# Optimization experiments

Hardware: AMD Instinct MI355X
Metric: run time of the kernel (lower is better)

Reference implementation:

```python
import jax, jax.numpy as jnp
import numpy as np

D_MODEL = 1024
NUM_HEADS = 16
HEAD_DIM = D_MODEL // NUM_HEADS

def setup_inputs() -> dict:
    key = jax.random.key(0)
    ks = jax.random.split(key, 9)
    B, L = 2, 2048
    s = 1.0 / np.sqrt(D_MODEL)
    return {
        "x":  jax.random.normal(ks[0], (B, L, D_MODEL), dtype=jnp.float32),
        "Wq": jax.random.uniform(ks[1], (D_MODEL, D_MODEL), jnp.float32, -s, s),
        "bq": jax.random.uniform(ks[2], (D_MODEL,), jnp.float32, -s, s),
        "Wk": jax.random.uniform(ks[3], (D_MODEL, D_MODEL), jnp.float32, -s, s),
        "bk": jax.random.uniform(ks[4], (D_MODEL,), jnp.float32, -s, s),
        "Wv": jax.random.uniform(ks[5], (D_MODEL, D_MODEL), jnp.float32, -s, s),
        "bv": jax.random.uniform(ks[6], (D_MODEL,), jnp.float32, -s, s),
        "Wo": jax.random.uniform(ks[7], (D_MODEL, D_MODEL), jnp.float32, -s, s),
        "bo": jax.random.uniform(ks[8], (D_MODEL,), jnp.float32, -s, s),
    }

def _split_heads(t):
    B, L, _ = t.shape
    return t.reshape(B, L, NUM_HEADS, HEAD_DIM).transpose(0, 2, 1, 3)  # [B,H,L,Dh]

def reference(x, Wq, bq, Wk, bk, Wv, bv, Wo, bo):
    # Linear projections (torch Linear: y = x @ W.T + b)
    Q = _split_heads(x @ Wq.T + bq)
    K = _split_heads(x @ Wk.T + bk)
    V = _split_heads(x @ Wv.T + bv)
    scale = 1.0 / jnp.sqrt(jnp.asarray(HEAD_DIM, dtype=x.dtype))
    scores = jnp.einsum('bhqd,bhkd->bhqk', Q, K) * scale  # [B,H,L,L]
    attn_weights = jax.nn.softmax(scores, axis=-1)
    ctx = jnp.einsum('bhqk,bhkd->bhqd', attn_weights, V)  # [B,H,L,Dh]
    B, H, L, Dh = ctx.shape
    ctx = ctx.transpose(0, 2, 1, 3).reshape(B, L, H * Dh)
    out = ctx @ Wo.T + bo  # dropout p=0.0 -> identity
    return (out, attn_weights)
```

## Files before the change

kernel.cpp:

```cpp
#include <hip/hip_runtime.h>

typedef unsigned short u16;
typedef __bf16 bf16x8 __attribute__((ext_vector_type(8)));
typedef float f32x4 __attribute__((ext_vector_type(4)));

#define WSTR 72
#define TSZ (64 * WSTR)

__device__ __forceinline__ u16 f2bf(float f) {
    union { float f; unsigned int u; } v; v.f = f;
    unsigned int u = v.u;
    u += 0x7fffu + ((u >> 16) & 1u);
    return (u16)(u >> 16);
}

__device__ __forceinline__ u16 cvt_bf(float f) {
    __bf16 h = (__bf16)f;
    union { __bf16 h; u16 u; } v; v.h = h; return v.u;
}

__device__ __forceinline__ void gload16(const u16* g, u16* l) {
    __builtin_amdgcn_global_load_lds((const __attribute__((address_space(1))) unsigned int*)(const void*)g,
                                     (__attribute__((address_space(3))) unsigned int*)(void*)l, 16, 0, 0);
}

#define MFMA16(A, B, C) __builtin_amdgcn_mfma_f32_16x16x32_bf16(A, B, C, 0, 0, 0)

#define LGKM_BARRIER() do { \
    asm volatile("s_waitcnt lgkmcnt(0)\n\ts_barrier" ::: "memory"); \
    __builtin_amdgcn_sched_barrier(0); \
} while (0)

__global__ __launch_bounds__(256) void k_cvtX(const float* __restrict__ src, u16* __restrict__ dst) {
    const size_t i = ((size_t)blockIdx.x * 256 + threadIdx.x) * 8;
    float4 v0 = *(const float4*)(src + i);
    float4 v1 = *(const float4*)(src + i + 4);
    u16 o[8];
    o[0] = f2bf(v0.x); o[1] = f2bf(v0.y); o[2] = f2bf(v0.z); o[3] = f2bf(v0.w);
    o[4] = f2bf(v1.x); o[5] = f2bf(v1.y); o[6] = f2bf(v1.z); o[7] = f2bf(v1.w);
    *(uint4*)(dst + i) = *(const uint4*)o;
}

__global__ __launch_bounds__(256) void k_cvtW(const float* __restrict__ w0, const float* __restrict__ w1,
                                              const float* __restrict__ w2, const float* __restrict__ w3,
                                              u16* __restrict__ dst) {
    const int z = blockIdx.z;
    const float* src = z == 0 ? w0 : z == 1 ? w1 : z == 2 ? w2 : w3;
    const size_t i = ((size_t)blockIdx.x * 256 + threadIdx.x) * 8;
    float4 v0 = *(const float4*)(src + i);
    float4 v1 = *(const float4*)(src + i + 4);
    u16 o[8];
    o[0] = f2bf(v0.x); o[1] = f2bf(v0.y); o[2] = f2bf(v0.z); o[3] = f2bf(v0.w);
    o[4] = f2bf(v1.x); o[5] = f2bf(v1.y); o[6] = f2bf(v1.z); o[7] = f2bf(v1.w);
    *(uint4*)(dst + (size_t)z * 1048576 + i) = *(const uint4*)o;
}

__global__ __launch_bounds__(256) void k_qkv(const u16* __restrict__ Xb, const u16* __restrict__ Wb,
                                             const float* __restrict__ bq, const float* __restrict__ bk,
                                             const float* __restrict__ bv,
                                             u16* __restrict__ Q, u16* __restrict__ Kd, u16* __restrict__ Vt) {
    __shared__ __align__(16) u16 lA[128 * 32];
    __shared__ __align__(16) u16 lB[128 * 32];
    __shared__ __align__(16) u16 lE[128 * 72];
    const int t = threadIdx.x;
    const int n0 = blockIdx.x * 128;
    const int m0 = blockIdx.y * 128;
    const int lane = t & 63, wave = t >> 6;
    const int wm = (wave >> 1) * 64, wn = (wave & 1) * 64;
    const int quad = lane >> 4, m16 = lane & 15;
    const int r4 = t >> 2, c8 = (t & 3) * 8;
    f32x4 acc[4][4] = {};
    for (int k0 = 0; k0 < 1024; k0 += 32) {
        gload16(Xb + (size_t)(m0 + r4) * 1024 + k0 + c8,       &lA[t * 8]);
        gload16(Xb + (size_t)(m0 + 64 + r4) * 1024 + k0 + c8,  &lA[2048 + t * 8]);
        gload16(Wb + (size_t)(n0 + r4) * 1024 + k0 + c8,       &lB[t * 8]);
        gload16(Wb + (size_t)(n0 + 64 + r4) * 1024 + k0 + c8,  &lB[2048 + t * 8]);
        __syncthreads();
        bf16x8 af[4], bfr[4];
#pragma unroll
        for (int i = 0; i < 4; ++i) {
            af[i]  = *(const bf16x8*)(lA + (wm + i * 16 + m16) * 32 + quad * 8);
            bfr[i] = *(const bf16x8*)(lB + (wn + i * 16 + m16) * 32 + quad * 8);
        }
#pragma unroll
        for (int mi = 0; mi < 4; ++mi)
#pragma unroll
            for (int ni = 0; ni < 4; ++ni)
                acc[mi][ni] = MFMA16(af[mi], bfr[ni], acc[mi][ni]);
        __syncthreads();
    }
    const int b = m0 >> 11, l0 = m0 & 2047;
#pragma unroll
    for (int hx = 0; hx < 2; ++hx) {
        __syncthreads();
        if ((wave & 1) == hx) {
#pragma unroll
            for (int ni = 0; ni < 4; ++ni) {
                const int col = n0 + wn + ni * 16 + m16;
                const int mat = col >> 10;
                const float bias = (mat == 0 ? bq : mat == 1 ? bk : bv)[col & 1023];
#pragma unroll
                for (int mi = 0; mi < 4; ++mi)
#pragma unroll
                    for (int e = 0; e < 4; ++e)
                        lE[(wm + mi * 16 + quad * 4 + e) * 72 + ni * 16 + m16] = cvt_bf(acc[mi][ni][e] + bias);
            }
        }
        __syncthreads();
        const int gb = n0 + hx * 64;
        const int mat = gb >> 10, h = (gb & 1023) >> 6;
        const int bh = b * 16 + h;
        if (mat < 2) {
            u16* dst = (mat == 0 ? Q : Kd) + (((size_t)bh * 2048) + l0) * 64;
            const int r = t >> 1, off = (t & 1) * 32;
            const u16* s = lE + r * 72 + off;
            u16* d2 = dst + (size_t)r * 64 + off;
            *(uint4*)(d2 + 0)  = *(const uint4*)(s + 0);
            *(uint4*)(d2 + 8)  = *(const uint4*)(s + 8);
            *(uint4*)(d2 + 16) = *(const uint4*)(s + 16);
            *(uint4*)(d2 + 24) = *(const uint4*)(s + 24);
        } else {
            const int d = t >> 2, ch = t & 3;
            u16* dst = Vt + ((size_t)bh * 64 + d) * 2048 + l0 + ch * 32;
#pragma unroll
            for (int seg = 0; seg < 4; ++seg) {
                u16 p[8];
#pragma unroll
                for (int j = 0; j < 8; ++j) p[j] = lE[(ch * 32 + seg * 8 + j) * 72 + d];
                *(uint4*)(dst + seg * 8) = *(const uint4*)p;
            }
        }
    }
}

__global__ __launch_bounds__(256) void k_attn(const u16* __restrict__ Q,
                                              const u16* __restrict__ K,
                                              const u16* __restrict__ Vt,
                                              float* __restrict__ attn,
                                              u16* __restrict__ ctx) {
    __shared__ __align__(16) u16 lK[2 * TSZ];
    __shared__ __align__(16) u16 lV[2 * TSZ];
    __shared__ __align__(16) u16 lW[2 * TSZ];
    __shared__ float sred[2][64];
    const int t = threadIdx.x;
    const int bh = blockIdx.x;
    const int m0 = blockIdx.y * 64;
    const int lane = t & 63, wave = t >> 6;
    const int wq = (wave & 1) * 32;
    const int wk = (wave >> 1) * 32;
    const int wm = (wave >> 1) * 32, wn = (wave & 1) * 32;
    const int quad = lane >> 4, m16 = lane & 15;
    const int sr = t >> 3, sc = (t & 7) * 8;
    const u16* Qh = Q + (size_t)bh * 2048 * 64;
    const u16* Kh = K + (size_t)bh * 2048 * 64;
    const u16* Vh = Vt + (size_t)bh * 64 * 2048;
    float* ah = attn + ((size_t)bh << 22) + (size_t)m0 * 2048;

    const float SC = 0.18033688011112042f;

    bf16x8 qf[2][2];
#pragma unroll
    for (int ni = 0; ni < 2; ++ni)
#pragma unroll
        for (int ks = 0; ks < 2; ++ks)
            qf[ni][ks] = *(const bf16x8*)(Qh + (size_t)(m0 + wq + ni * 16 + m16) * 64 + ks * 32 + quad * 8);

    float slane[2] = {0.f, 0.f};
    {
        *(uint4*)&lK[sr * WSTR + sc]        = *(const uint4*)(Kh + (size_t)sr * 64 + sc);
        *(uint4*)&lK[(sr + 32) * WSTR + sc] = *(const uint4*)(Kh + (size_t)(sr + 32) * 64 + sc);
        int buf = 0;
        for (int kt = 0; kt < 32; ++kt) {
            LGKM_BARRIER();
            uint4 kr0, kr1;
            if (kt < 31) {
                const u16* kp = Kh + (size_t)(kt + 1) * 64 * 64;
                kr0 = *(const uint4*)(kp + (size_t)sr * 64 + sc);
                kr1 = *(const uint4*)(kp + (size_t)(sr + 32) * 64 + sc);
            }
            const u16* lKb = &lK[buf * TSZ];
            bf16x8 k00 = *(const bf16x8*)(lKb + (wk + m16) * WSTR + quad * 8);
            bf16x8 k01 = *(const bf16x8*)(lKb + (wk + m16) * WSTR + 32 + quad * 8);
            bf16x8 k10 = *(const bf16x8*)(lKb + (wk + 16 + m16) * WSTR + quad * 8);
            bf16x8 k11 = *(const bf16x8*)(lKb + (wk + 16 + m16) * WSTR + 32 + quad * 8);
            f32x4 sacc[2][2] = {};
            __builtin_amdgcn_s_setprio(1);
            sacc[0][0] = MFMA16(k00, qf[0][0], sacc[0][0]);
            sacc[0][1] = MFMA16(k00, qf[1][0], sacc[0][1]);
            sacc[1][0] = MFMA16(k10, qf[0][0], sacc[1][0]);
            sacc[1][1] = MFMA16(k10, qf[1][0], sacc[1][1]);
            sacc[0][0] = MFMA16(k01, qf[0][1], sacc[0][0]);
            sacc[0][1] = MFMA16(k01, qf[1][1], sacc[0][1]);
            sacc[1][0] = MFMA16(k11, qf[0][1], sacc[1][0]);
            sacc[1][1] = MFMA16(k11, qf[1][1], sacc[1][1]);
            __builtin_amdgcn_s_setprio(0);
#pragma unroll
            for (int mi = 0; mi < 2; ++mi)
#pragma unroll
                for (int e = 0; e < 4; ++e) {
                    slane[0] += __builtin_amdgcn_exp2f(sacc[mi][0][e] * SC);
                    slane[1] += __builtin_amdgcn_exp2f(sacc[mi][1][e] * SC);
                }
            if (kt < 31) {
                u16* dK = &lK[(buf ^ 1) * TSZ];
                *(uint4*)&dK[sr * WSTR + sc]        = kr0;
                *(uint4*)&dK[(sr + 32) * WSTR + sc] = kr1;
            }
            buf ^= 1;
        }
    }
#pragma unroll
    for (int ni = 0; ni < 2; ++ni) {
        slane[ni] += __shfl_xor(slane[ni], 16);
        slane[ni] += __shfl_xor(slane[ni], 32);
    }
    __syncthreads();
    if (quad == 0) {
        sred[wave >> 1][wq + m16]      = slane[0];
        sred[wave >> 1][wq + 16 + m16] = slane[1];
    }
    __syncthreads();
    float inv[2];
    inv[0] = 1.0f / (sred[0][wq + m16]      + sred[1][wq + m16]);
    inv[1] = 1.0f / (sred[0][wq + 16 + m16] + sred[1][wq + 16 + m16]);

    unsigned aoff[2][2], lwoff[2][2];
#pragma unroll
    for (int mi = 0; mi < 2; ++mi)
#pragma unroll
        for (int ni = 0; ni < 2; ++ni) {
            const int q = wq + ni * 16 + m16;
            const int k = wk + mi * 16 + quad * 4;
            aoff[mi][ni]  = (unsigned)(q * 2048 + k);
            lwoff[mi][ni] = (unsigned)(q * WSTR + k);
        }

    f32x4 cacc[2][2] = {};
    bf16x8 vp00 = {}, vp01 = {}, vp10 = {}, vp11 = {};
    {
        *(uint4*)&lK[sr * WSTR + sc]        = *(const uint4*)(Kh + (size_t)sr * 64 + sc);
        *(uint4*)&lK[(sr + 32) * WSTR + sc] = *(const uint4*)(Kh + (size_t)(sr + 32) * 64 + sc);
        *(uint4*)&lV[sr * WSTR + sc]        = *(const uint4*)(Vh + (size_t)sr * 2048 + sc);
        *(uint4*)&lV[(sr + 32) * WSTR + sc] = *(const uint4*)(Vh + (size_t)(sr + 32) * 2048 + sc);
        int buf = 0;
        for (int kt = 0; kt < 32; ++kt) {
            LGKM_BARRIER();
            uint4 kr0, kr1, vr0, vr1;
            if (kt < 31) {
                const u16* kp  = Kh + (size_t)(kt + 1) * 64 * 64;
                const u16* vp2 = Vh + (size_t)(kt + 1) * 64;
                kr0 = *(const uint4*)(kp + (size_t)sr * 64 + sc);
                kr1 = *(const uint4*)(kp + (size_t)(sr + 32) * 64 + sc);
                vr0 = *(const uint4*)(vp2 + (size_t)sr * 2048 + sc);
                vr1 = *(const uint4*)(vp2 + (size_t)(sr + 32) * 2048 + sc);
            }
            const u16* lKb = &lK[buf * TSZ];
            const u16* lVb = &lV[buf * TSZ];
            bf16x8 vn00 = *(const bf16x8*)(lVb + (wn + m16) * WSTR + quad * 8);
            bf16x8 vn01 = *(const bf16x8*)(lVb + (wn + m16) * WSTR + 32 + quad * 8);
            bf16x8 vn10 = *(const bf16x8*)(lVb + (wn + 16 + m16) * WSTR + quad * 8);
            bf16x8 vn11 = *(const bf16x8*)(lVb + (wn + 16 + m16) * WSTR + 32 + quad * 8);
            bf16x8 k00 = *(const bf16x8*)(lKb + (wk + m16) * WSTR + quad * 8);
            bf16x8 k01 = *(const bf16x8*)(lKb + (wk + m16) * WSTR + 32 + quad * 8);
            bf16x8 k10 = *(const bf16x8*)(lKb + (wk + 16 + m16) * WSTR + quad * 8);
            bf16x8 k11 = *(const bf16x8*)(lKb + (wk + 16 + m16) * WSTR + 32 + quad * 8);
            f32x4 sacc[2][2] = {};
            __builtin_amdgcn_s_setprio(1);
            sacc[0][0] = MFMA16(k00, qf[0][0], sacc[0][0]);
            sacc[0][1] = MFMA16(k00, qf[1][0], sacc[0][1]);
            sacc[1][0] = MFMA16(k10, qf[0][0], sacc[1][0]);
            sacc[1][1] = MFMA16(k10, qf[1][0], sacc[1][1]);
            sacc[0][0] = MFMA16(k01, qf[0][1], sacc[0][0]);
            sacc[0][1] = MFMA16(k01, qf[1][1], sacc[0][1]);
            sacc[1][0] = MFMA16(k11, qf[0][1], sacc[1][0]);
            sacc[1][1] = MFMA16(k11, qf[1][1], sacc[1][1]);
            __builtin_amdgcn_s_setprio(0);
#pragma unroll
            for (int mi = 0; mi < 2; ++mi)
#pragma unroll
                for (int ni = 0; ni < 2; ++ni)
#pragma unroll
                    for (int e = 0; e < 4; ++e)
                        sacc[mi][ni][e] = __builtin_amdgcn_exp2f(sacc[mi][ni][e] * SC) * inv[ni];
            u16* lwb = &lW[(kt & 1) * TSZ];
#pragma unroll
            for (int mi = 0; mi < 2; ++mi)
#pragma unroll
                for (int ni = 0; ni < 2; ++ni) {
                    u16 p[4];
                    p[0] = cvt_bf(sacc[mi][ni][0]); p[1] = cvt_bf(sacc[mi][ni][1]);
                    p[2] = cvt_bf(sacc[mi][ni][2]); p[3] = cvt_bf(sacc[mi][ni][3]);
                    *(uint2*)&lwb[lwoff[mi][ni]] = *(const uint2*)p;
                }
            float* ap = ah + kt * 64;
#pragma unroll
            for (int mi = 0; mi < 2; ++mi)
#pragma unroll
                for (int ni = 0; ni < 2; ++ni)
                    *(f32x4*)(ap + aoff[mi][ni]) = sacc[mi][ni];
            if (kt < 31) {
                u16* dK = &lK[(buf ^ 1) * TSZ];
                u16* dV = &lV[(buf ^ 1) * TSZ];
                *(uint4*)&dK[sr * WSTR + sc]        = kr0;
                *(uint4*)&dK[(sr + 32) * WSTR + sc] = kr1;
                *(uint4*)&dV[sr * WSTR + sc]        = vr0;
                *(uint4*)&dV[(sr + 32) * WSTR + sc] = vr1;
            }
            if (kt > 0) {
                const u16* lwp = &lW[((kt - 1) & 1) * TSZ];
                bf16x8 a00 = *(const bf16x8*)(lwp + (wm + m16) * WSTR + quad * 8);
                bf16x8 a01 = *(const bf16x8*)(lwp + (wm + m16) * WSTR + 32 + quad * 8);
                bf16x8 a10 = *(const bf16x8*)(lwp + (wm + 16 + m16) * WSTR + quad * 8);
                bf16x8 a11 = *(const bf16x8*)(lwp + (wm + 16 + m16) * WSTR + 32 + quad * 8);
                __builtin_amdgcn_s_setprio(1);
                cacc[0][0] = MFMA16(a00, vp00, cacc[0][0]);
                cacc[0][1] = MFMA16(a00, vp10, cacc[0][1]);
                cacc[1][0] = MFMA16(a10, vp00, cacc[1][0]);
                cacc[1][1] = MFMA16(a10, vp10, cacc[1][1]);
                cacc[0][0] = MFMA16(a01, vp01, cacc[0][0]);
                cacc[0][1] = MFMA16(a01, vp11, cacc[0][1]);
                cacc[1][0] = MFMA16(a11, vp01, cacc[1][0]);
                cacc[1][1] = MFMA16(a11, vp11, cacc[1][1]);
                __builtin_amdgcn_s_setprio(0);
            }
            vp00 = vn00; vp01 = vn01; vp10 = vn10; vp11 = vn11;
            buf ^= 1;
        }
        __syncthreads();
        const u16* lwp = &lW[(31 & 1) * TSZ];
        bf16x8 a00 = *(const bf16x8*)(lwp + (wm + m16) * WSTR + quad * 8);
        bf16x8 a01 = *(const bf16x8*)(lwp + (wm + m16) * WSTR + 32 + quad * 8);
        bf16x8 a10 = *(const bf16x8*)(lwp + (wm + 16 + m16) * WSTR + quad * 8);
        bf16x8 a11 = *(const bf16x8*)(lwp + (wm + 16 + m16) * WSTR + 32 + quad * 8);
        cacc[0][0] = MFMA16(a00, vp00, cacc[0][0]);
        cacc[0][1] = MFMA16(a00, vp10, cacc[0][1]);
        cacc[1][0] = MFMA16(a10, vp00, cacc[1][0]);
        cacc[1][1] = MFMA16(a10, vp10, cacc[1][1]);
        cacc[0][0] = MFMA16(a01, vp01, cacc[0][0]);
        cacc[0][1] = MFMA16(a01, vp11, cacc[0][1]);
        cacc[1][0] = MFMA16(a11, vp01, cacc[1][0]);
        cacc[1][1] = MFMA16(a11, vp11, cacc[1][1]);
    }

    const int b = bh >> 4, h = bh & 15;
    u16* cp = ctx + ((size_t)b * 2048) * 1024 + h * 64;
#pragma unroll
    for (int mi = 0; mi < 2; ++mi)
#pragma unroll
        for (int ni = 0; ni < 2; ++ni)
#pragma unroll
            for (int e = 0; e < 4; ++e) {
                const int row = m0 + wm + mi * 16 + quad * 4 + e;
                const int col = wn + ni * 16 + m16;
                cp[(size_t)row * 1024 + col] = cvt_bf(cacc[mi][ni][e]);
            }
}

__global__ __launch_bounds__(256) void k_out(const u16* __restrict__ ctx,
                                             const u16* __restrict__ WoB,
                                             const float* __restrict__ bo,
                                             float* __restrict__ out) {
    __shared__ __align__(16) u16 lA[128 * 32];
    __shared__ __align__(16) u16 lB[128 * 32];
    const int t = threadIdx.x;
    const int n0 = blockIdx.x * 128;
    const int m0 = blockIdx.y * 128;
    const int lane = t & 63, wave = t >> 6;
    const int wm = (wave >> 1) * 64, wn = (wave & 1) * 64;
    const int quad = lane >> 4, m16 = lane & 15;
    const int r4 = t >> 2, c8 = (t & 3) * 8;
    f32x4 acc[4][4] = {};
    for (int k0 = 0; k0 < 1024; k0 += 32) {
        gload16(ctx + (size_t)(m0 + r4) * 1024 + k0 + c8,       &lA[t * 8]);
        gload16(ctx + (size_t)(m0 + 64 + r4) * 1024 + k0 + c8,  &lA[2048 + t * 8]);
        gload16(WoB + (size_t)(n0 + r4) * 1024 + k0 + c8,       &lB[t * 8]);
        gload16(WoB + (size_t)(n0 + 64 + r4) * 1024 + k0 + c8,  &lB[2048 + t * 8]);
        __syncthreads();
        bf16x8 af[4], bfr[4];
#pragma unroll
        for (int i = 0; i < 4; ++i) {
            af[i]  = *(const bf16x8*)(lA + (wm + i * 16 + m16) * 32 + quad * 8);
            bfr[i] = *(const bf16x8*)(lB + (wn + i * 16 + m16) * 32 + quad * 8);
        }
#pragma unroll
        for (int mi = 0; mi < 4; ++mi)
#pragma unroll
            for (int ni = 0; ni < 4; ++ni)
                acc[mi][ni] = MFMA16(af[mi], bfr[ni], acc[mi][ni]);
        __syncthreads();
    }
#pragma unroll
    for (int ni = 0; ni < 4; ++ni) {
        const int col = n0 + wn + ni * 16 + m16;
        const float bv = bo[col];
#pragma unroll
        for (int mi = 0; mi < 4; ++mi)
#pragma unroll
            for (int e = 0; e < 4; ++e) {
                const int row = m0 + wm + mi * 16 + quad * 4 + e;
                out[(size_t)row * 1024 + col] = acc[mi][ni][e] + bv;
            }
    }
}

extern "C" void kernel_launch(void* const* d_in, const int* in_sizes, int n_in,
                              void* d_out, int out_size, void* d_ws, size_t ws_size,
                              hipStream_t stream) {
    const float* x  = (const float*)d_in[0];
    const float* Wq = (const float*)d_in[1];
    const float* bq = (const float*)d_in[2];
    const float* Wk = (const float*)d_in[3];
    const float* bk = (const float*)d_in[4];
    const float* Wv = (const float*)d_in[5];
    const float* bv = (const float*)d_in[6];
    const float* Wo = (const float*)d_in[7];
    const float* bo = (const float*)d_in[8];

    float* out_f = (float*)d_out;
    float* attn  = out_f + (size_t)4096 * 1024;

    u16* Xb = (u16*)d_ws;
    u16* Wb = Xb + (size_t)4194304;
    u16* Qb = Wb + (size_t)4194304;
    u16* Kb = Qb + (size_t)4194304;
    u16* Vt = Kb + (size_t)4194304;

    dim3 blk(256);
    k_cvtX<<<dim3(2048), blk, 0, stream>>>(x, Xb);
    k_cvtW<<<dim3(512, 1, 4), blk, 0, stream>>>(Wq, Wk, Wv, Wo, Wb);
    k_qkv<<<dim3(24, 32), blk, 0, stream>>>(Xb, Wb, bq, bk, bv, Qb, Kb, Vt);
    k_attn<<<dim3(32, 32), blk, 0, stream>>>(Qb, Kb, Vt, attn, Xb);
    k_out<<<dim3(8, 32), blk, 0, stream>>>(Xb, Wb + (size_t)3072 * 1024, bo, out_f);
}
```

Baseline: 702.5 us.

## Split softmax row-sum pass into separate kernel with larger key tiles

Moves the first pass of attention (computing the exp row sums) out of the attention kernel into its own kernel, which gives each wave 64 query rows and 32 keys per 128-key tile so K loads are reused across more queries and fewer loop iterations are needed. The inverse sums are written to a scratch region in the output buffer, reusing the out area that k_out later overwrites, and the second kernel reads them back. The second kernel also drops the s_setprio hints around its MFMA blocks. The cost is an extra kernel launch plus a small global round trip for the normalizers, and the second kernel's smaller shared-memory footprint may change occupancy.

```diff
diff --git a/kernel.cpp b/kernel.cpp
--- a/kernel.cpp
+++ b/kernel.cpp
@@ -6,6 +6,7 @@
 
 #define WSTR 72
 #define TSZ (64 * WSTR)
+#define KTSZ (128 * WSTR)
 
 __device__ __forceinline__ u16 f2bf(float f) {
     union { float f; unsigned int u; } v; v.f = f;
@@ -133,15 +134,99 @@
     }
 }
 
-__global__ __launch_bounds__(256) void k_attn(const u16* __restrict__ Q,
-                                              const u16* __restrict__ K,
-                                              const u16* __restrict__ Vt,
-                                              float* __restrict__ attn,
-                                              u16* __restrict__ ctx) {
+__global__ __launch_bounds__(256) void k_sum(const u16* __restrict__ Q,
+                                             const u16* __restrict__ K,
+                                             float* __restrict__ invg) {
+    __shared__ __align__(16) u16 lK[2 * KTSZ];
+    __shared__ float sred[4][64];
+    const int t = threadIdx.x;
+    const int bh = blockIdx.x;
+    const int m0 = blockIdx.y * 64;
+    const int lane = t & 63, wave = t >> 6;
+    const int wk = wave * 32;
+    const int quad = lane >> 4, m16 = lane & 15;
+    const int sr = t >> 3, sc = (t & 7) * 8;
+    const u16* Qh = Q + (size_t)bh * 2048 * 64;
+    const u16* Kh = K + (size_t)bh * 2048 * 64;
+    const float SC = 0.18033688011112042f;
+
+    bf16x8 qf[4][2];
+#pragma unroll
+    for (int ni = 0; ni < 4; ++ni)
+#pragma unroll
+        for (int ks = 0; ks < 2; ++ks)
+            qf[ni][ks] = *(const bf16x8*)(Qh + (size_t)(m0 + ni * 16 + m16) * 64 + ks * 32 + quad * 8);
+
+    float slane[4] = {0.f, 0.f, 0.f, 0.f};
+#pragma unroll
+    for (int g = 0; g < 4; ++g)
+        *(uint4*)&lK[(sr + g * 32) * WSTR + sc] = *(const uint4*)(Kh + (size_t)(sr + g * 32) * 64 + sc);
+    int buf = 0;
+    for (int kt = 0; kt < 16; ++kt) {
+        LGKM_BARRIER();
+        uint4 kr[4];
+        if (kt < 15) {
+            const u16* kp = Kh + (size_t)(kt + 1) * 128 * 64;
+#pragma unroll
+            for (int g = 0; g < 4; ++g)
+                kr[g] = *(const uint4*)(kp + (size_t)(sr + g * 32) * 64 + sc);
+        }
+        const u16* lKb = &lK[buf * KTSZ];
+        bf16x8 kf[2][2];
+#pragma unroll
+        for (int mi = 0; mi < 2; ++mi)
+#pragma unroll
+            for (int ks = 0; ks < 2; ++ks)
+                kf[mi][ks] = *(const bf16x8*)(lKb + (wk + mi * 16 + m16) * WSTR + ks * 32 + quad * 8);
+        f32x4 sacc[2][4] = {};
+#pragma unroll
+        for (int ks = 0; ks < 2; ++ks)
+#pragma unroll
+            for (int ni = 0; ni < 4; ++ni) {
+                sacc[0][ni] = MFMA16(kf[0][ks], qf[ni][ks], sacc[0][ni]);
+                sacc[1][ni] = MFMA16(kf[1][ks], qf[ni][ks], sacc[1][ni]);
+            }
+#pragma unroll
+        for (int ni = 0; ni < 4; ++ni)
+#pragma unroll
+            for (int mi = 0; mi < 2; ++mi)
+#pragma unroll
+                for (int e = 0; e < 4; ++e)
+                    slane[ni] += __builtin_amdgcn_exp2f(sacc[mi][ni][e] * SC);
+        if (kt < 15) {
+            u16* dK = &lK[(buf ^ 1) * KTSZ];
+#pragma unroll
+            for (int g = 0; g < 4; ++g)
+                *(uint4*)&dK[(sr + g * 32) * WSTR + sc] = kr[g];
+        }
+        buf ^= 1;
+    }
+#pragma unroll
+    for (int ni = 0; ni < 4; ++ni) {
+        slane[ni] += __shfl_xor(slane[ni], 16);
+        slane[ni] += __shfl_xor(slane[ni], 32);
+    }
+    if (quad == 0) {
+#pragma unroll
+        for (int ni = 0; ni < 4; ++ni)
+            sred[wave][ni * 16 + m16] = slane[ni];
+    }
+    __syncthreads();
+    if (t < 64) {
+        const float s = (sred[0][t] + sred[1][t]) + (sred[2][t] + sred[3][t]);
+        invg[(size_t)bh * 2048 + m0 + t] = 1.0f / s;
+    }
+}
+
+__global__ __launch_bounds__(256) void k_wpv(const u16* __restrict__ Q,
+                                             const u16* __restrict__ K,
+                                             const u16* __restrict__ Vt,
+                                             const float* __restrict__ invg,
+                                             float* __restrict__ attn,
+                                             u16* __restrict__ ctx) {
     __shared__ __align__(16) u16 lK[2 * TSZ];
     __shared__ __align__(16) u16 lV[2 * TSZ];
     __shared__ __align__(16) u16 lW[2 * TSZ];
-    __shared__ float sred[2][64];
     const int t = threadIdx.x;
     const int bh = blockIdx.x;
     const int m0 = blockIdx.y * 64;
@@ -155,7 +240,6 @@
     const u16* Kh = K + (size_t)bh * 2048 * 64;
     const u16* Vh = Vt + (size_t)bh * 64 * 2048;
     float* ah = attn + ((size_t)bh << 22) + (size_t)m0 * 2048;
-
     const float SC = 0.18033688011112042f;
 
     bf16x8 qf[2][2];
@@ -165,64 +249,9 @@
         for (int ks = 0; ks < 2; ++ks)
             qf[ni][ks] = *(const bf16x8*)(Qh + (size_t)(m0 + wq + ni * 16 + m16) * 64 + ks * 32 + quad * 8);
 
-    float slane[2] = {0.f, 0.f};
-    {
-        *(uint4*)&lK[sr * WSTR + sc]        = *(const uint4*)(Kh + (size_t)sr * 64 + sc);
-        *(uint4*)&lK[(sr + 32) * WSTR + sc] = *(const uint4*)(Kh + (size_t)(sr + 32) * 64 + sc);
-        int buf = 0;
-        for (int kt = 0; kt < 32; ++kt) {
-            LGKM_BARRIER();
-            uint4 kr0, kr1;
-            if (kt < 31) {
-                const u16* kp = Kh + (size_t)(kt + 1) * 64 * 64;
-                kr0 = *(const uint4*)(kp + (size_t)sr * 64 + sc);
-                kr1 = *(const uint4*)(kp + (size_t)(sr + 32) * 64 + sc);
-            }
-            const u16* lKb = &lK[buf * TSZ];
-            bf16x8 k00 = *(const bf16x8*)(lKb + (wk + m16) * WSTR + quad * 8);
-            bf16x8 k01 = *(const bf16x8*)(lKb + (wk + m16) * WSTR + 32 + quad * 8);
-            bf16x8 k10 = *(const bf16x8*)(lKb + (wk + 16 + m16) * WSTR + quad * 8);
-            bf16x8 k11 = *(const bf16x8*)(lKb + (wk + 16 + m16) * WSTR + 32 + quad * 8);
-            f32x4 sacc[2][2] = {};
-            __builtin_amdgcn_s_setprio(1);
-            sacc[0][0] = MFMA16(k00, qf[0][0], sacc[0][0]);
-            sacc[0][1] = MFMA16(k00, qf[1][0], sacc[0][1]);
-            sacc[1][0] = MFMA16(k10, qf[0][0], sacc[1][0]);
-            sacc[1][1] = MFMA16(k10, qf[1][0], sacc[1][1]);
-            sacc[0][0] = MFMA16(k01, qf[0][1], sacc[0][0]);
-            sacc[0][1] = MFMA16(k01, qf[1][1], sacc[0][1]);
-            sacc[1][0] = MFMA16(k11, qf[0][1], sacc[1][0]);
-            sacc[1][1] = MFMA16(k11, qf[1][1], sacc[1][1]);
-            __builtin_amdgcn_s_setprio(0);
-#pragma unroll
-            for (int mi = 0; mi < 2; ++mi)
-#pragma unroll
-                for (int e = 0; e < 4; ++e) {
-                    slane[0] += __builtin_amdgcn_exp2f(sacc[mi][0][e] * SC);
-                    slane[1] += __builtin_amdgcn_exp2f(sacc[mi][1][e] * SC);
-                }
-            if (kt < 31) {
-                u16* dK = &lK[(buf ^ 1) * TSZ];
-                *(uint4*)&dK[sr * WSTR + sc]        = kr0;
-                *(uint4*)&dK[(sr + 32) * WSTR + sc] = kr1;
-            }
-            buf ^= 1;
-        }
-    }
-#pragma unroll
-    for (int ni = 0; ni < 2; ++ni) {
-        slane[ni] += __shfl_xor(slane[ni], 16);
-        slane[ni] += __shfl_xor(slane[ni], 32);
-    }
-    __syncthreads();
-    if (quad == 0) {
-        sred[wave >> 1][wq + m16]      = slane[0];
-        sred[wave >> 1][wq + 16 + m16] = slane[1];
-    }
-    __syncthreads();
     float inv[2];
-    inv[0] = 1.0f / (sred[0][wq + m16]      + sred[1][wq + m16]);
-    inv[1] = 1.0f / (sred[0][wq + 16 + m16] + sred[1][wq + 16 + m16]);
+    inv[0] = invg[(size_t)bh * 2048 + m0 + wq + m16];
+    inv[1] = invg[(size_t)bh * 2048 + m0 + wq + 16 + m16];
 
     unsigned aoff[2][2], lwoff[2][2];
 #pragma unroll
@@ -265,7 +294,6 @@
             bf16x8 k10 = *(const bf16x8*)(lKb + (wk + 16 + m16) * WSTR + quad * 8);
             bf16x8 k11 = *(const bf16x8*)(lKb + (wk + 16 + m16) * WSTR + 32 + quad * 8);
             f32x4 sacc[2][2] = {};
-            __builtin_amdgcn_s_setprio(1);
             sacc[0][0] = MFMA16(k00, qf[0][0], sacc[0][0]);
             sacc[0][1] = MFMA16(k00, qf[1][0], sacc[0][1]);
             sacc[1][0] = MFMA16(k10, qf[0][0], sacc[1][0]);
@@ -274,7 +302,6 @@
             sacc[0][1] = MFMA16(k01, qf[1][1], sacc[0][1]);
             sacc[1][0] = MFMA16(k11, qf[0][1], sacc[1][0]);
             sacc[1][1] = MFMA16(k11, qf[1][1], sacc[1][1]);
-            __builtin_amdgcn_s_setprio(0);
 #pragma unroll
             for (int mi = 0; mi < 2; ++mi)
 #pragma unroll
@@ -312,7 +339,6 @@
                 bf16x8 a01 = *(const bf16x8*)(lwp + (wm + m16) * WSTR + 32 + quad * 8);
                 bf16x8 a10 = *(const bf16x8*)(lwp + (wm + 16 + m16) * WSTR + quad * 8);
                 bf16x8 a11 = *(const bf16x8*)(lwp + (wm + 16 + m16) * WSTR + 32 + quad * 8);
-                __builtin_amdgcn_s_setprio(1);
                 cacc[0][0] = MFMA16(a00, vp00, cacc[0][0]);
                 cacc[0][1] = MFMA16(a00, vp10, cacc[0][1]);
                 cacc[1][0] = MFMA16(a10, vp00, cacc[1][0]);
@@ -321,7 +347,6 @@
                 cacc[0][1] = MFMA16(a01, vp11, cacc[0][1]);
                 cacc[1][0] = MFMA16(a11, vp01, cacc[1][0]);
                 cacc[1][1] = MFMA16(a11, vp11, cacc[1][1]);
-                __builtin_amdgcn_s_setprio(0);
             }
             vp00 = vn00; vp01 = vn01; vp10 = vn10; vp11 = vn11;
             buf ^= 1;
@@ -418,6 +443,7 @@
 
     float* out_f = (float*)d_out;
     float* attn  = out_f + (size_t)4096 * 1024;
+    float* invg  = out_f;
 
     u16* Xb = (u16*)d_ws;
     u16* Wb = Xb + (size_t)4194304;
@@ -429,6 +455,7 @@
     k_cvtX<<<dim3(2048), blk, 0, stream>>>(x, Xb);
     k_cvtW<<<dim3(512, 1, 4), blk, 0, stream>>>(Wq, Wk, Wv, Wo, Wb);
     k_qkv<<<dim3(24, 32), blk, 0, stream>>>(Xb, Wb, bq, bk, bv, Qb, Kb, Vt);
-    k_attn<<<dim3(32, 32), blk, 0, stream>>>(Qb, Kb, Vt, attn, Xb);
+    k_sum<<<dim3(32, 32), blk, 0, stream>>>(Qb, Kb, invg);
+    k_wpv<<<dim3(32, 32), blk, 0, stream>>>(Qb, Kb, Vt, invg, attn, Xb);
     k_out<<<dim3(8, 32), blk, 0, stream>>>(Xb, Wb + (size_t)3072 * 1024, bo, out_f);
 }
```

Measured after the change: 714.8 us. Within noise of the previous version (+1.8%).

## Stage K/V tiles via direct global-to-LDS loads with XOR-swizzled layout

Applied to the files above, without the earlier changes.

Replaces register-staged K and V tile copies in the attention kernel with global_load_lds direct-to-LDS loads into an unpadded buffer. Bank conflicts are avoided by XOR-swizzling the column index instead of padding. Barriers now wait on vmcnt, with vmcnt(8) in the second pass so the outstanding attention-weight stores need not drain. The s_setprio hints around MFMA blocks are removed. This removes VGPR staging and the extra ds_write instructions, at the cost of relying on correct vmcnt accounting for the store and load ordering.

```diff
diff --git a/kernel.cpp b/kernel.cpp
--- a/kernel.cpp
+++ b/kernel.cpp
@@ -6,6 +6,9 @@
 
 #define WSTR 72
 #define TSZ (64 * WSTR)
+#define KBUF 4096
+
+#define SWZ(r, e) ((r) * 64 + ((e) ^ (((r) & 7) * 8)))
 
 __device__ __forceinline__ u16 f2bf(float f) {
     union { float f; unsigned int u; } v; v.f = f;
@@ -26,8 +29,12 @@
 
 #define MFMA16(A, B, C) __builtin_amdgcn_mfma_f32_16x16x32_bf16(A, B, C, 0, 0, 0)
 
-#define LGKM_BARRIER() do { \
-    asm volatile("s_waitcnt lgkmcnt(0)\n\ts_barrier" ::: "memory"); \
+#define BAR_V0() do { \
+    asm volatile("s_waitcnt vmcnt(0) lgkmcnt(0)\n\ts_barrier" ::: "memory"); \
+    __builtin_amdgcn_sched_barrier(0); \
+} while (0)
+#define BAR_V8() do { \
+    asm volatile("s_waitcnt vmcnt(8) lgkmcnt(0)\n\ts_barrier" ::: "memory"); \
     __builtin_amdgcn_sched_barrier(0); \
 } while (0)
 
@@ -138,8 +145,8 @@
                                               const u16* __restrict__ Vt,
                                               float* __restrict__ attn,
                                               u16* __restrict__ ctx) {
-    __shared__ __align__(16) u16 lK[2 * TSZ];
-    __shared__ __align__(16) u16 lV[2 * TSZ];
+    __shared__ __align__(16) u16 lK[2 * KBUF];
+    __shared__ __align__(16) u16 lV[2 * KBUF];
     __shared__ __align__(16) u16 lW[2 * TSZ];
     __shared__ float sred[2][64];
     const int t = threadIdx.x;
@@ -150,13 +157,18 @@
     const int wk = (wave >> 1) * 32;
     const int wm = (wave >> 1) * 32, wn = (wave & 1) * 32;
     const int quad = lane >> 4, m16 = lane & 15;
-    const int sr = t >> 3, sc = (t & 7) * 8;
     const u16* Qh = Q + (size_t)bh * 2048 * 64;
     const u16* Kh = K + (size_t)bh * 2048 * 64;
     const u16* Vh = Vt + (size_t)bh * 64 * 2048;
     float* ah = attn + ((size_t)bh << 22) + (size_t)m0 * 2048;
-
     const float SC = 0.18033688011112042f;
+
+    const int sr2 = t >> 3, su = t & 7;
+    const int lu = su ^ (sr2 & 7);
+    const u16* Ksrc0 = Kh + (size_t)sr2 * 64 + lu * 8;
+    const u16* Ksrc1 = Kh + (size_t)(sr2 + 32) * 64 + lu * 8;
+    const u16* Vsrc0 = Vh + (size_t)sr2 * 2048 + lu * 8;
+    const u16* Vsrc1 = Vh + (size_t)(sr2 + 32) * 2048 + lu * 8;
 
     bf16x8 qf[2][2];
 #pragma unroll
@@ -167,24 +179,22 @@
 
     float slane[2] = {0.f, 0.f};
     {
-        *(uint4*)&lK[sr * WSTR + sc]        = *(const uint4*)(Kh + (size_t)sr * 64 + sc);
-        *(uint4*)&lK[(sr + 32) * WSTR + sc] = *(const uint4*)(Kh + (size_t)(sr + 32) * 64 + sc);
+        gload16(Ksrc0, &lK[t * 8]);
+        gload16(Ksrc1, &lK[2048 + t * 8]);
         int buf = 0;
         for (int kt = 0; kt < 32; ++kt) {
-            LGKM_BARRIER();
-            uint4 kr0, kr1;
+            BAR_V0();
             if (kt < 31) {
-                const u16* kp = Kh + (size_t)(kt + 1) * 64 * 64;
-                kr0 = *(const uint4*)(kp + (size_t)sr * 64 + sc);
-                kr1 = *(const uint4*)(kp + (size_t)(sr + 32) * 64 + sc);
-            }
-            const u16* lKb = &lK[buf * TSZ];
-            bf16x8 k00 = *(const bf16x8*)(lKb + (wk + m16) * WSTR + quad * 8);
-            bf16x8 k01 = *(const bf16x8*)(lKb + (wk + m16) * WSTR + 32 + quad * 8);
-            bf16x8 k10 = *(const bf16x8*)(lKb + (wk + 16 + m16) * WSTR + quad * 8);
-            bf16x8 k11 = *(const bf16x8*)(lKb + (wk + 16 + m16) * WSTR + 32 + quad * 8);
+                u16* dK = &lK[(buf ^ 1) * KBUF];
+                gload16(Ksrc0 + (size_t)(kt + 1) * 4096, &dK[t * 8]);
+                gload16(Ksrc1 + (size_t)(kt + 1) * 4096, &dK[2048 + t * 8]);
+            }
+            const u16* lKb = &lK[buf * KBUF];
+            bf16x8 k00 = *(const bf16x8*)(lKb + SWZ(wk + m16,      quad * 8));
+            bf16x8 k01 = *(const bf16x8*)(lKb + SWZ(wk + m16,      32 + quad * 8));
+            bf16x8 k10 = *(const bf16x8*)(lKb + SWZ(wk + 16 + m16, quad * 8));
+            bf16x8 k11 = *(const bf16x8*)(lKb + SWZ(wk + 16 + m16, 32 + quad * 8));
             f32x4 sacc[2][2] = {};
-            __builtin_amdgcn_s_setprio(1);
             sacc[0][0] = MFMA16(k00, qf[0][0], sacc[0][0]);
             sacc[0][1] = MFMA16(k00, qf[1][0], sacc[0][1]);
             sacc[1][0] = MFMA16(k10, qf[0][0], sacc[1][0]);
@@ -193,7 +203,6 @@
             sacc[0][1] = MFMA16(k01, qf[1][1], sacc[0][1]);
             sacc[1][0] = MFMA16(k11, qf[0][1], sacc[1][0]);
             sacc[1][1] = MFMA16(k11, qf[1][1], sacc[1][1]);
-            __builtin_amdgcn_s_setprio(0);
 #pragma unroll
             for (int mi = 0; mi < 2; ++mi)
 #pragma unroll
@@ -201,11 +210,6 @@
                     slane[0] += __builtin_amdgcn_exp2f(sacc[mi][0][e] * SC);
                     slane[1] += __builtin_amdgcn_exp2f(sacc[mi][1][e] * SC);
                 }
-            if (kt < 31) {
-                u16* dK = &lK[(buf ^ 1) * TSZ];
-                *(uint4*)&dK[sr * WSTR + sc]        = kr0;
-                *(uint4*)&dK[(sr + 32) * WSTR + sc] = kr1;
-            }
             buf ^= 1;
         }
     }
@@ -238,34 +242,33 @@
     f32x4 cacc[2][2] = {};
     bf16x8 vp00 = {}, vp01 = {}, vp10 = {}, vp11 = {};
     {
-        *(uint4*)&lK[sr * WSTR + sc]        = *(const uint4*)(Kh + (size_t)sr * 64 + sc);
-        *(uint4*)&lK[(sr + 32) * WSTR + sc] = *(const uint4*)(Kh + (size_t)(sr + 32) * 64 + sc);
-        *(uint4*)&lV[sr * WSTR + sc]        = *(const uint4*)(Vh + (size_t)sr * 2048 + sc);
-        *(uint4*)&lV[(sr + 32) * WSTR + sc] = *(const uint4*)(Vh + (size_t)(sr + 32) * 2048 + sc);
+        gload16(Ksrc0, &lK[t * 8]);
+        gload16(Ksrc1, &lK[2048 + t * 8]);
+        gload16(Vsrc0, &lV[t * 8]);
+        gload16(Vsrc1, &lV[2048 + t * 8]);
+        asm volatile("s_waitcnt vmcnt(0)" ::: "memory");
         int buf = 0;
         for (int kt = 0; kt < 32; ++kt) {
-            LGKM_BARRIER();
-            uint4 kr0, kr1, vr0, vr1;
+            BAR_V8();
             if (kt < 31) {
-                const u16* kp  = Kh + (size_t)(kt + 1) * 64 * 64;
-                const u16* vp2 = Vh + (size_t)(kt + 1) * 64;
-                kr0 = *(const uint4*)(kp + (size_t)sr * 64 + sc);
-                kr1 = *(const uint4*)(kp + (size_t)(sr + 32) * 64 + sc);
-                vr0 = *(const uint4*)(vp2 + (size_t)sr * 2048 + sc);
-                vr1 = *(const uint4*)(vp2 + (size_t)(sr + 32) * 2048 + sc);
-            }
-            const u16* lKb = &lK[buf * TSZ];
-            const u16* lVb = &lV[buf * TSZ];
-            bf16x8 vn00 = *(const bf16x8*)(lVb + (wn + m16) * WSTR + quad * 8);
-            bf16x8 vn01 = *(const bf16x8*)(lVb + (wn + m16) * WSTR + 32 + quad * 8);
-            bf16x8 vn10 = *(const bf16x8*)(lVb + (wn + 16 + m16) * WSTR + quad * 8);
-            bf16x8 vn11 = *(const bf16x8*)(lVb + (wn + 16 + m16) * WSTR + 32 + quad * 8);
-            bf16x8 k00 = *(const bf16x8*)(lKb + (wk + m16) * WSTR + quad * 8);
-            bf16x8 k01 = *(const bf16x8*)(lKb + (wk + m16) * WSTR + 32 + quad * 8);
-            bf16x8 k10 = *(const bf16x8*)(lKb + (wk + 16 + m16) * WSTR + quad * 8);
-            bf16x8 k11 = *(const bf16x8*)(lKb + (wk + 16 + m16) * WSTR + 32 + quad * 8);
+                u16* dK = &lK[(buf ^ 1) * KBUF];
+                u16* dV = &lV[(buf ^ 1) * KBUF];
+                gload16(Ksrc0 + (size_t)(kt + 1) * 4096, &dK[t * 8]);
+                gload16(Ksrc1 + (size_t)(kt + 1) * 4096, &dK[2048 + t * 8]);
+                gload16(Vsrc0 + (size_t)(kt + 1) * 64,   &dV[t * 8]);
+                gload16(Vsrc1 + (size_t)(kt + 1) * 64,   &dV[2048 + t * 8]);
+            }
+            const u16* lKb = &lK[buf * KBUF];
+            const u16* lVb = &lV[buf * KBUF];
+            bf16x8 vn00 = *(const bf16x8*)(lVb + SWZ(wn + m16,      quad * 8));
+            bf16x8 vn01 = *(const bf16x8*)(lVb + SWZ(wn + m16,      32 + quad * 8));
+            bf16x8 vn10 = *(const bf16x8*)(lVb + SWZ(wn + 16 + m16, quad * 8));
+            bf16x8 vn11 = *(const bf16x8*)(lVb + SWZ(wn + 16 + m16, 32 + quad * 8));
+            bf16x8 k00 = *(const bf16x8*)(lKb + SWZ(wk + m16,      quad * 8));
+            bf16x8 k01 = *(const bf16x8*)(lKb + SWZ(wk + m16,      32 + quad * 8));
+            bf16x8 k10 = *(const bf16x8*)(lKb + SWZ(wk + 16 + m16, quad * 8));
+            bf16x8 k11 = *(const bf16x8*)(lKb + SWZ(wk + 16 + m16, 32 + quad * 8));
             f32x4 sacc[2][2] = {};
-            __builtin_amdgcn_s_setprio(1);
             sacc[0][0] = MFMA16(k00, qf[0][0], sacc[0][0]);
             sacc[0][1] = MFMA16(k00, qf[1][0], sacc[0][1]);
             sacc[1][0] = MFMA16(k10, qf[0][0], sacc[1][0]);
@@ -274,7 +277,6 @@
             sacc[0][1] = MFMA16(k01, qf[1][1], sacc[0][1]);
             sacc[1][0] = MFMA16(k11, qf[0][1], sacc[1][0]);
             sacc[1][1] = MFMA16(k11, qf[1][1], sacc[1][1]);
-            __builtin_amdgcn_s_setprio(0);
 #pragma unroll
             for (int mi = 0; mi < 2; ++mi)
 #pragma unroll
@@ -298,21 +300,12 @@
 #pragma unroll
                 for (int ni = 0; ni < 2; ++ni)
                     *(f32x4*)(ap + aoff[mi][ni]) = sacc[mi][ni];
-            if (kt < 31) {
-                u16* dK = &lK[(buf ^ 1) * TSZ];
-                u16* dV = &lV[(buf ^ 1) * TSZ];
-                *(uint4*)&dK[sr * WSTR + sc]        = kr0;
-                *(uint4*)&dK[(sr + 32) * WSTR + sc] = kr1;
-                *(uint4*)&dV[sr * WSTR + sc]        = vr0;
-                *(uint4*)&dV[(sr + 32) * WSTR + sc] = vr1;
-            }
             if (kt > 0) {
                 const u16* lwp = &lW[((kt - 1) & 1) * TSZ];
                 bf16x8 a00 = *(const bf16x8*)(lwp + (wm + m16) * WSTR + quad * 8);
                 bf16x8 a01 = *(const bf16x8*)(lwp + (wm + m16) * WSTR + 32 + quad * 8);
                 bf16x8 a10 = *(const bf16x8*)(lwp + (wm + 16 + m16) * WSTR + quad * 8);
                 bf16x8 a11 = *(const bf16x8*)(lwp + (wm + 16 + m16) * WSTR + 32 + quad * 8);
-                __builtin_amdgcn_s_setprio(1);
                 cacc[0][0] = MFMA16(a00, vp00, cacc[0][0]);
                 cacc[0][1] = MFMA16(a00, vp10, cacc[0][1]);
                 cacc[1][0] = MFMA16(a10, vp00, cacc[1][0]);
@@ -321,7 +314,6 @@
                 cacc[0][1] = MFMA16(a01, vp11, cacc[0][1]);
                 cacc[1][0] = MFMA16(a11, vp01, cacc[1][0]);
                 cacc[1][1] = MFMA16(a11, vp11, cacc[1][1]);
-                __builtin_amdgcn_s_setprio(0);
             }
             vp00 = vn00; vp01 = vn01; vp10 = vn10; vp11 = vn11;
             buf ^= 1;
```

New measurement: 745.1 us. +6.1%, slower.
